# Performance work log

Measured on AMD Instinct MI355X. Metric: run time of the kernel, lower is better.

## Reference

```python
import jax, jax.numpy as jnp
import numpy as np

N_NODES = 100000
N_EDGES = 1600000
IN_FEATS = 512
HIDDEN = 128
N_CLASSES = 2
N_LAYERS = 2
NEG_SLOPE = 0.01  # F.leaky_relu default


def setup_inputs() -> dict:
    key = jax.random.key(0)
    ks = jax.random.split(key, 12)
    features = jax.random.normal(ks[0], (N_NODES, IN_FEATS), dtype=jnp.float32)
    src = jax.random.randint(ks[1], (N_EDGES,), 0, N_NODES, dtype=jnp.int32)
    dst = jax.random.randint(ks[2], (N_EDGES,), 0, N_NODES, dtype=jnp.int32)
    # params (torch Linear convention: W is [out, in], y = x @ W.T + b)
    s_in = 1.0 / np.sqrt(IN_FEATS)
    s_h = 1.0 / np.sqrt(HIDDEN)
    W_in = jax.random.uniform(ks[3], (HIDDEN, IN_FEATS), jnp.float32, -s_in, s_in)
    b_in = jax.random.uniform(ks[4], (HIDDEN,), jnp.float32, -s_in, s_in)
    # SAGEConv per layer: fc_self (with bias) + fc_neigh (no bias), stacked over layers
    W_self = jax.random.uniform(ks[5], (N_LAYERS, HIDDEN, HIDDEN), jnp.float32, -s_h, s_h)
    b_self = jax.random.uniform(ks[6], (N_LAYERS, HIDDEN), jnp.float32, -s_h, s_h)
    W_neigh = jax.random.uniform(ks[7], (N_LAYERS, HIDDEN, HIDDEN), jnp.float32, -s_h, s_h)
    W_out = jax.random.uniform(ks[8], (N_CLASSES, HIDDEN), jnp.float32, -s_h, s_h)
    b_out = jax.random.uniform(ks[9], (N_CLASSES,), jnp.float32, -s_h, s_h)
    return {
        "features": features, "src": src, "dst": dst,
        "W_in": W_in, "b_in": b_in,
        "W_self": W_self, "b_self": b_self, "W_neigh": W_neigh,
        "W_out": W_out, "b_out": b_out,
    }


def reference(features, src, dst, W_in, b_in, W_self, b_self, W_neigh, W_out, b_out):
    # input projection (dropout is identity in eval / p=0)
    h = features @ W_in.T + b_in  # [N, H]
    # in-degree for mean aggregation (zero-degree nodes -> zero neighbor feat)
    deg = jax.ops.segment_sum(jnp.ones((src.shape[0],), h.dtype), dst,
                              num_segments=N_NODES)
    inv_deg = (1.0 / jnp.maximum(deg, 1.0))[:, None]  # [N, 1]
    for l in range(N_LAYERS):
        # mean over in-neighbors: scatter-add h[src] onto dst, divide by degree
        h_neigh = jax.ops.segment_sum(h[src], dst, num_segments=N_NODES) * inv_deg
        h = h @ W_self[l].T + b_self[l] + h_neigh @ W_neigh[l].T
        h = jax.nn.leaky_relu(h, negative_slope=NEG_SLOPE)
    return h @ W_out.T + b_out  # [N, n_classes]
```

## Files before the change

### kernel.cpp

```cpp
#include <hip/hip_runtime.h>


#define N_NODES 100000
#define N_EDGES 1600000
#define IN_FEATS 512
#define HIDDEN 128
#define NEG_SLOPE 0.01f
#define SCAN_BLOCKS 49

#define N_RANGES 8
#define RANGE_SZ 12500
#define FILL_CHUNKS 256
#define FILL_CHUNK 6250

typedef __attribute__((ext_vector_type(8))) __bf16 bf16x8;
typedef __attribute__((ext_vector_type(4))) float f32x4;
typedef __attribute__((ext_vector_type(8))) _Float16 half8;

__global__ __launch_bounds__(256) void k_degree(const int* __restrict__ dst,
                                                int* __restrict__ deg) {
  int r = blockIdx.x & 7;
  int c = blockIdx.x >> 3;
  int lo = r * RANGE_SZ, hi = lo + RANGE_SZ;
  int e0 = c * FILL_CHUNK;
  int e1 = e0 + FILL_CHUNK;
  if (e1 > N_EDGES) e1 = N_EDGES;
  for (int e = e0 + threadIdx.x; e < e1; e += 256) {
    int d = dst[e];
    if (d >= lo && d < hi) atomicAdd(&deg[d], 1);
  }
}

__device__ __forceinline__ int wave_incl_scan(int v) {
  #pragma unroll
  for (int d = 1; d < 64; d <<= 1) {
    int t = __shfl_up(v, d, 64);
    if ((threadIdx.x & 63) >= d) v += t;
  }
  return v;
}

__global__ __launch_bounds__(256) void k_scanA(const int* __restrict__ deg,
                                               int* __restrict__ out,
                                               int* __restrict__ bsums) {
  __shared__ int wsum[4];
  int base = blockIdx.x * 2048 + threadIdx.x * 8;
  int v[8];
  int s = 0;
  #pragma unroll
  for (int i = 0; i < 8; i++) {
    int idx = base + i;
    v[i] = (idx < N_NODES) ? deg[idx] : 0;
    s += v[i];
  }
  int incl = wave_incl_scan(s);
  int wid = threadIdx.x >> 6;
  if ((threadIdx.x & 63) == 63) wsum[wid] = incl;
  __syncthreads();
  int woff = 0;
  #pragma unroll
  for (int w = 0; w < 4; w++)
    if (w < wid) woff += wsum[w];
  int run = woff + incl - s;
  #pragma unroll
  for (int i = 0; i < 8; i++) {
    int idx = base + i;
    if (idx < N_NODES) out[idx] = run;
    run += v[i];
  }
  if (threadIdx.x == 255) bsums[blockIdx.x] = woff + incl;
}

__global__ __launch_bounds__(64) void k_scanB(const int* __restrict__ bsums,
                                              int* __restrict__ boffs) {
  int t = threadIdx.x;
  int v = (t < SCAN_BLOCKS) ? bsums[t] : 0;
  int incl = wave_incl_scan(v);
  if (t < SCAN_BLOCKS) boffs[t] = incl - v;
}

__global__ __launch_bounds__(256) void k_scanC(const int* __restrict__ deg,
                                               int* __restrict__ row_start,
                                               int* __restrict__ cursor,
                                               float* __restrict__ inv_deg,
                                               const int* __restrict__ boffs) {
  int b = boffs[blockIdx.x];
  int base = blockIdx.x * 2048 + threadIdx.x * 8;
  #pragma unroll
  for (int i = 0; i < 8; i++) {
    int idx = base + i;
    if (idx < N_NODES) {
      int rs = row_start[idx] + b;
      row_start[idx] = rs;
      cursor[idx] = rs;
      int d = deg[idx];
      inv_deg[idx] = 1.0f / (float)(d > 1 ? d : 1);
    }
  }
  if (blockIdx.x == 0 && threadIdx.x == 0) row_start[N_NODES] = N_EDGES;
}

__global__ __launch_bounds__(256) void k_fill(const int* __restrict__ src,
                                              const int* __restrict__ dst,
                                              int* __restrict__ cursor,
                                              int* __restrict__ csr_src) {
  int r = blockIdx.x & 7;
  int c = blockIdx.x >> 3;
  int lo = r * RANGE_SZ, hi = lo + RANGE_SZ;
  int e0 = c * FILL_CHUNK;
  int e1 = e0 + FILL_CHUNK;
  if (e1 > N_EDGES) e1 = N_EDGES;
  for (int e = e0 + threadIdx.x; e < e1; e += 256) {
    int d = dst[e];
    if (d >= lo && d < hi) {
      int p = atomicAdd(&cursor[d], 1);
      csr_src[p] = src[e];
    }
  }
}

template <int K1, int K2, bool RELU, bool WF16>
__global__ __launch_bounds__(256) void k_gemm(const float* __restrict__ A1,
                                              const float* __restrict__ A2,
                                              const float* __restrict__ W1,
                                              const float* __restrict__ W2,
                                              const float* __restrict__ bias,
                                              float* __restrict__ C,
                                              _Float16* __restrict__ C16) {
  constexpr int BK = 32;
  constexpr int KT = (K1 + K2) / BK;
  constexpr int LP = 40;
  __shared__ __bf16 As_h[128 * LP];
  __shared__ __bf16 As_l[128 * LP];
  __shared__ __bf16 Bs_h[128 * LP];
  __shared__ __bf16 Bs_l[128 * LP];

  const int tid = threadIdx.x;
  const int lane = tid & 63;
  const int wid = tid >> 6;
  const int wr = wid >> 1;
  const int wc = wid & 1;
  const int lr = lane & 15;
  const int kg = lane >> 4;
  const int r0 = blockIdx.x * 128;

  f32x4 acc[4][4];
  #pragma unroll
  for (int m = 0; m < 4; m++)
    #pragma unroll
    for (int n = 0; n < 4; n++) acc[m][n] = (f32x4){0.f, 0.f, 0.f, 0.f};

  float4 ra[4], rb[4];

  auto load_tile = [&](int kt) {
    const float* Ap;
    const float* Wp;
    int k0, lda;
    if (K2 == 0 || kt * BK < K1) {
      Ap = A1; Wp = W1; k0 = kt * BK; lda = K1;
    } else {
      Ap = A2; Wp = W2; k0 = kt * BK - K1; lda = K2;
    }
    #pragma unroll
    for (int i = 0; i < 4; i++) {
      int flat = i * 256 + tid;
      int row = flat >> 3;
      int q = flat & 7;
      int gr = r0 + row;
      ra[i] = (gr < N_NODES) ? *(const float4*)&Ap[(long)gr * lda + k0 + q * 4]
                             : make_float4(0.f, 0.f, 0.f, 0.f);
      rb[i] = *(const float4*)&Wp[(long)row * lda + k0 + q * 4];
    }
  };

  auto split_write = [&](float v, __bf16* hp, __bf16* lp, int off) {
    __bf16 h = (__bf16)v;
    float rem = v - (float)h;
    hp[off] = h;
    lp[off] = (__bf16)rem;
  };

  load_tile(0);

  for (int kt = 0; kt < KT; ++kt) {
    if (kt > 0) __syncthreads();
    #pragma unroll
    for (int i = 0; i < 4; i++) {
      int flat = i * 256 + tid;
      int row = flat >> 3;
      int q = flat & 7;
      int off = row * LP + q * 4;
      split_write(ra[i].x, As_h, As_l, off + 0);
      split_write(ra[i].y, As_h, As_l, off + 1);
      split_write(ra[i].z, As_h, As_l, off + 2);
      split_write(ra[i].w, As_h, As_l, off + 3);
      split_write(rb[i].x, Bs_h, Bs_l, off + 0);
      split_write(rb[i].y, Bs_h, Bs_l, off + 1);
      split_write(rb[i].z, Bs_h, Bs_l, off + 2);
      split_write(rb[i].w, Bs_h, Bs_l, off + 3);
    }
    __syncthreads();
    if (kt + 1 < KT) load_tile(kt + 1);

    bf16x8 ah[4], al[4];
    #pragma unroll
    for (int m = 0; m < 4; m++) {
      int arow = wr * 64 + m * 16 + lr;
      ah[m] = *(const bf16x8*)&As_h[arow * LP + kg * 8];
      al[m] = *(const bf16x8*)&As_l[arow * LP + kg * 8];
    }
    #pragma unroll
    for (int n = 0; n < 4; n++) {
      int bcol = wc * 64 + n * 16 + lr;
      bf16x8 bh = *(const bf16x8*)&Bs_h[bcol * LP + kg * 8];
      bf16x8 bl = *(const bf16x8*)&Bs_l[bcol * LP + kg * 8];
      #pragma unroll
      for (int m = 0; m < 4; m++) {
        acc[m][n] = __builtin_amdgcn_mfma_f32_16x16x32_bf16(ah[m], bh, acc[m][n], 0, 0, 0);
        acc[m][n] = __builtin_amdgcn_mfma_f32_16x16x32_bf16(al[m], bh, acc[m][n], 0, 0, 0);
        acc[m][n] = __builtin_amdgcn_mfma_f32_16x16x32_bf16(ah[m], bl, acc[m][n], 0, 0, 0);
      }
    }
  }

  #pragma unroll
  for (int n = 0; n < 4; n++) {
    int col = wc * 64 + n * 16 + lr;
    float bc = bias[col];
    #pragma unroll
    for (int m = 0; m < 4; m++) {
      int rowb = r0 + wr * 64 + m * 16 + kg * 4;
      #pragma unroll
      for (int j = 0; j < 4; j++) {
        int row = rowb + j;
        if (row < N_NODES) {
          float v = acc[m][n][j] + bc;
          if (RELU) v = v > 0.f ? v : v * NEG_SLOPE;
          C[(long)row * 128 + col] = v;
          if (WF16) C16[(long)row * 128 + col] = (_Float16)v;
        }
      }
    }
  }
}

__global__ __launch_bounds__(256) void k_agg(const _Float16* __restrict__ h16,
                                             const int* __restrict__ row_start,
                                             const int* __restrict__ csr_src,
                                             const float* __restrict__ inv_deg,
                                             float* __restrict__ hn) {
  int node = blockIdx.x * 16 + (threadIdx.x >> 4);
  int lane = threadIdx.x & 15;
  int s = row_start[node];
  int e = row_start[node + 1];
  float acc[8];
  #pragma unroll
  for (int j = 0; j < 8; j++) acc[j] = 0.f;

  int i = s;
  for (; i + 4 <= e; i += 4) {
    int s0 = csr_src[i + 0];
    int s1 = csr_src[i + 1];
    int s2 = csr_src[i + 2];
    int s3 = csr_src[i + 3];
    half8 v0 = *(const half8*)&h16[(long)s0 * HIDDEN + lane * 8];
    half8 v1 = *(const half8*)&h16[(long)s1 * HIDDEN + lane * 8];
    half8 v2 = *(const half8*)&h16[(long)s2 * HIDDEN + lane * 8];
    half8 v3 = *(const half8*)&h16[(long)s3 * HIDDEN + lane * 8];
    #pragma unroll
    for (int j = 0; j < 8; j++)
      acc[j] += ((float)v0[j] + (float)v1[j]) + ((float)v2[j] + (float)v3[j]);
  }
  for (; i < e; ++i) {
    int sn = csr_src[i];
    half8 v = *(const half8*)&h16[(long)sn * HIDDEN + lane * 8];
    #pragma unroll
    for (int j = 0; j < 8; j++) acc[j] += (float)v[j];
  }

  float id = inv_deg[node];
  float4 o0, o1;
  o0.x = acc[0] * id; o0.y = acc[1] * id; o0.z = acc[2] * id; o0.w = acc[3] * id;
  o1.x = acc[4] * id; o1.y = acc[5] * id; o1.z = acc[6] * id; o1.w = acc[7] * id;
  *(float4*)&hn[(long)node * HIDDEN + lane * 8 + 0] = o0;
  *(float4*)&hn[(long)node * HIDDEN + lane * 8 + 4] = o1;
}

__global__ __launch_bounds__(256) void k_out(const float* __restrict__ h,
                                             const float* __restrict__ W_out,
                                             const float* __restrict__ b_out,
                                             float* __restrict__ out) {
  int node = blockIdx.x * 4 + (threadIdx.x >> 6);
  int l = threadIdx.x & 63;
  float a = h[node * HIDDEN + l];
  float b = h[node * HIDDEN + 64 + l];
  float s0 = a * W_out[l] + b * W_out[64 + l];
  float s1 = a * W_out[128 + l] + b * W_out[192 + l];
  #pragma unroll
  for (int d = 32; d >= 1; d >>= 1) {
    s0 += __shfl_xor(s0, d, 64);
    s1 += __shfl_xor(s1, d, 64);
  }
  if (l == 0) {
    out[node * 2 + 0] = s0 + b_out[0];
    out[node * 2 + 1] = s1 + b_out[1];
  }
}

extern "C" void kernel_launch(void* const* d_in, const int* in_sizes, int n_in,
                              void* d_out, int out_size, void* d_ws, size_t ws_size,
                              hipStream_t stream) {
  const float* features = (const float*)d_in[0];
  const int* src = (const int*)d_in[1];
  const int* dst = (const int*)d_in[2];
  const float* W_in = (const float*)d_in[3];
  const float* b_in = (const float*)d_in[4];
  const float* W_self = (const float*)d_in[5];
  const float* b_self = (const float*)d_in[6];
  const float* W_neigh = (const float*)d_in[7];
  const float* W_out = (const float*)d_in[8];
  const float* b_out = (const float*)d_in[9];
  float* out = (float*)d_out;

  char* ws = (char*)d_ws;
  float* h = (float*)(ws + 0);
  float* hn = (float*)(ws + 51200000);
  int* deg = (int*)(ws + 102400000);
  float* inv_deg = (float*)(ws + 102800000);
  int* row_start = (int*)(ws + 103200000);
  int* cursor = (int*)(ws + 103600016);
  int* csr_src = (int*)(ws + 104000016);
  int* bsums = (int*)(ws + 110400016);
  int* boffs = (int*)(ws + 110400272);
  _Float16* h16 = (_Float16*)(ws + 110401024);

  hipMemsetAsync(deg, 0, N_NODES * sizeof(int), stream);
  k_degree<<<N_RANGES * FILL_CHUNKS, 256, 0, stream>>>(dst, deg);
  k_scanA<<<SCAN_BLOCKS, 256, 0, stream>>>(deg, row_start, bsums);
  k_scanB<<<1, 64, 0, stream>>>(bsums, boffs);
  k_scanC<<<SCAN_BLOCKS, 256, 0, stream>>>(deg, row_start, cursor, inv_deg, boffs);
  k_fill<<<N_RANGES * FILL_CHUNKS, 256, 0, stream>>>(src, dst, cursor, csr_src);

  k_gemm<IN_FEATS, 0, false, true><<<782, 256, 0, stream>>>(
      features, nullptr, W_in, nullptr, b_in, h, h16);

  k_agg<<<6250, 256, 0, stream>>>(h16, row_start, csr_src, inv_deg, hn);
  k_gemm<HIDDEN, HIDDEN, true, true><<<782, 256, 0, stream>>>(
      h, hn, W_self, W_neigh, b_self, h, h16);

  k_agg<<<6250, 256, 0, stream>>>(h16, row_start, csr_src, inv_deg, hn);
  k_gemm<HIDDEN, HIDDEN, true, false><<<782, 256, 0, stream>>>(
      h, hn, W_self + HIDDEN * HIDDEN, W_neigh + HIDDEN * HIDDEN,
      b_self + HIDDEN, h, nullptr);

  k_out<<<25000, 256, 0, stream>>>(h, W_out, b_out, out);
}
```

Baseline: 722.7 us.

## Pre-split weights and activations into bf16 hi/lo and load MFMA fragments directly

Measured after the change: 870.1 us. 1.2x slower.

```diff
diff --git a/kernel.cpp b/kernel.cpp
--- a/kernel.cpp
+++ b/kernel.cpp
@@ -14,6 +14,7 @@
 #define FILL_CHUNK 6250
 
 typedef __attribute__((ext_vector_type(8))) __bf16 bf16x8;
+typedef __attribute__((ext_vector_type(4))) __bf16 bf16x4;
 typedef __attribute__((ext_vector_type(4))) float f32x4;
 typedef __attribute__((ext_vector_type(8))) _Float16 half8;
 
@@ -119,108 +120,122 @@
   }
 }
 
-template <int K1, int K2, bool RELU, bool WF16>
-__global__ __launch_bounds__(256) void k_gemm(const float* __restrict__ A1,
-                                              const float* __restrict__ A2,
-                                              const float* __restrict__ W1,
-                                              const float* __restrict__ W2,
-                                              const float* __restrict__ bias,
-                                              float* __restrict__ C,
-                                              _Float16* __restrict__ C16) {
+__global__ __launch_bounds__(256) void k_split(const float* __restrict__ in,
+                                               __bf16* __restrict__ hi,
+                                               __bf16* __restrict__ lo, int n) {
+  int i = (blockIdx.x * 256 + threadIdx.x) * 4;
+  if (i >= n) return;
+  float4 v = *(const float4*)&in[i];
+  float vv[4] = {v.x, v.y, v.z, v.w};
+  bf16x4 h4, l4;
+  #pragma unroll
+  for (int j = 0; j < 4; j++) {
+    __bf16 hh = (__bf16)vv[j];
+    h4[j] = hh;
+    l4[j] = (__bf16)(vv[j] - (float)hh);
+  }
+  *(bf16x4*)&hi[i] = h4;
+  *(bf16x4*)&lo[i] = l4;
+}
+
+template <int K1, int K2, bool RELU, bool A16, bool WF32, bool WSPLIT, bool WF16>
+__global__ __launch_bounds__(256, 2) void k_gemm(
+    const void* __restrict__ A1a, const void* __restrict__ A1b,
+    const void* __restrict__ A2a, const void* __restrict__ A2b,
+    const __bf16* __restrict__ W1h, const __bf16* __restrict__ W1l,
+    const __bf16* __restrict__ W2h, const __bf16* __restrict__ W2l,
+    const float* __restrict__ bias,
+    float* __restrict__ Cf, __bf16* __restrict__ Ch, __bf16* __restrict__ Cl,
+    _Float16* __restrict__ C16) {
+  static_assert(K2 == 0 || K2 == K1, "uniform lda required");
   constexpr int BK = 32;
   constexpr int KT = (K1 + K2) / BK;
-  constexpr int LP = 40;
-  __shared__ __bf16 As_h[128 * LP];
-  __shared__ __bf16 As_l[128 * LP];
-  __shared__ __bf16 Bs_h[128 * LP];
-  __shared__ __bf16 Bs_l[128 * LP];
-
   const int tid = threadIdx.x;
   const int lane = tid & 63;
   const int wid = tid >> 6;
-  const int wr = wid >> 1;
-  const int wc = wid & 1;
-  const int lr = lane & 15;
-  const int kg = lane >> 4;
+  const int wr = wid >> 1, wc = wid & 1;
+  const int lr = lane & 15, kg = lane >> 4;
   const int r0 = blockIdx.x * 128;
 
+  long abase[4];
+  long bbase[4];
+  #pragma unroll
+  for (int m = 0; m < 4; m++) {
+    int r = r0 + wr * 64 + m * 16 + lr;
+    int rc = (r < N_NODES) ? r : (N_NODES - 1);
+    abase[m] = (long)rc * K1;
+    bbase[m] = (long)(wc * 64 + m * 16 + lr) * K1;
+  }
+
   f32x4 acc[4][4];
   #pragma unroll
   for (int m = 0; m < 4; m++)
     #pragma unroll
     for (int n = 0; n < 4; n++) acc[m][n] = (f32x4){0.f, 0.f, 0.f, 0.f};
 
-  float4 ra[4], rb[4];
-
-  auto load_tile = [&](int kt) {
-    const float* Ap;
-    const float* Wp;
-    int k0, lda;
-    if (K2 == 0 || kt * BK < K1) {
-      Ap = A1; Wp = W1; k0 = kt * BK; lda = K1;
+  float4 af[4][2];
+  bf16x8 sah[4], sal[4];
+  bf16x8 sbh[4], sbl[4];
+  bf16x8 ah[4], al[4], bh[4], bl[4];
+
+  auto issue = [&](int kt) {
+    const bool fst = (K2 == 0) || (kt * BK < K1);
+    const int k0 = (fst ? kt * BK : kt * BK - K1) + kg * 8;
+    if constexpr (A16) {
+      const __bf16* Ah = (const __bf16*)(fst ? A1a : A2a);
+      const __bf16* Al = (const __bf16*)(fst ? A1b : A2b);
+      #pragma unroll
+      for (int m = 0; m < 4; m++) {
+        sah[m] = *(const bf16x8*)&Ah[abase[m] + k0];
+        sal[m] = *(const bf16x8*)&Al[abase[m] + k0];
+      }
     } else {
-      Ap = A2; Wp = W2; k0 = kt * BK - K1; lda = K2;
-    }
-    #pragma unroll
-    for (int i = 0; i < 4; i++) {
-      int flat = i * 256 + tid;
-      int row = flat >> 3;
-      int q = flat & 7;
-      int gr = r0 + row;
-      ra[i] = (gr < N_NODES) ? *(const float4*)&Ap[(long)gr * lda + k0 + q * 4]
-                             : make_float4(0.f, 0.f, 0.f, 0.f);
-      rb[i] = *(const float4*)&Wp[(long)row * lda + k0 + q * 4];
+      const float* Af = (const float*)(fst ? A1a : A2a);
+      #pragma unroll
+      for (int m = 0; m < 4; m++) {
+        af[m][0] = *(const float4*)&Af[abase[m] + k0];
+        af[m][1] = *(const float4*)&Af[abase[m] + k0 + 4];
+      }
+    }
+    const __bf16* Bh = fst ? W1h : W2h;
+    const __bf16* Bl = fst ? W1l : W2l;
+    #pragma unroll
+    for (int n = 0; n < 4; n++) {
+      sbh[n] = *(const bf16x8*)&Bh[bbase[n] + k0];
+      sbl[n] = *(const bf16x8*)&Bl[bbase[n] + k0];
     }
   };
 
-  auto split_write = [&](float v, __bf16* hp, __bf16* lp, int off) {
-    __bf16 h = (__bf16)v;
-    float rem = v - (float)h;
-    hp[off] = h;
-    lp[off] = (__bf16)rem;
-  };
-
-  load_tile(0);
-
+  issue(0);
+  #pragma unroll 4
   for (int kt = 0; kt < KT; ++kt) {
-    if (kt > 0) __syncthreads();
-    #pragma unroll
-    for (int i = 0; i < 4; i++) {
-      int flat = i * 256 + tid;
-      int row = flat >> 3;
-      int q = flat & 7;
-      int off = row * LP + q * 4;
-      split_write(ra[i].x, As_h, As_l, off + 0);
-      split_write(ra[i].y, As_h, As_l, off + 1);
-      split_write(ra[i].z, As_h, As_l, off + 2);
-      split_write(ra[i].w, As_h, As_l, off + 3);
-      split_write(rb[i].x, Bs_h, Bs_l, off + 0);
-      split_write(rb[i].y, Bs_h, Bs_l, off + 1);
-      split_write(rb[i].z, Bs_h, Bs_l, off + 2);
-      split_write(rb[i].w, Bs_h, Bs_l, off + 3);
-    }
-    __syncthreads();
-    if (kt + 1 < KT) load_tile(kt + 1);
-
-    bf16x8 ah[4], al[4];
-    #pragma unroll
-    for (int m = 0; m < 4; m++) {
-      int arow = wr * 64 + m * 16 + lr;
-      ah[m] = *(const bf16x8*)&As_h[arow * LP + kg * 8];
-      al[m] = *(const bf16x8*)&As_l[arow * LP + kg * 8];
-    }
-    #pragma unroll
-    for (int n = 0; n < 4; n++) {
-      int bcol = wc * 64 + n * 16 + lr;
-      bf16x8 bh = *(const bf16x8*)&Bs_h[bcol * LP + kg * 8];
-      bf16x8 bl = *(const bf16x8*)&Bs_l[bcol * LP + kg * 8];
+    if constexpr (A16) {
+      #pragma unroll
+      for (int m = 0; m < 4; m++) { ah[m] = sah[m]; al[m] = sal[m]; }
+    } else {
       #pragma unroll
       for (int m = 0; m < 4; m++) {
-        acc[m][n] = __builtin_amdgcn_mfma_f32_16x16x32_bf16(ah[m], bh, acc[m][n], 0, 0, 0);
-        acc[m][n] = __builtin_amdgcn_mfma_f32_16x16x32_bf16(al[m], bh, acc[m][n], 0, 0, 0);
-        acc[m][n] = __builtin_amdgcn_mfma_f32_16x16x32_bf16(ah[m], bl, acc[m][n], 0, 0, 0);
+        float v[8] = {af[m][0].x, af[m][0].y, af[m][0].z, af[m][0].w,
+                      af[m][1].x, af[m][1].y, af[m][1].z, af[m][1].w};
+        #pragma unroll
+        for (int j = 0; j < 8; j++) {
+          __bf16 hh = (__bf16)v[j];
+          ah[m][j] = hh;
+          al[m][j] = (__bf16)(v[j] - (float)hh);
+        }
       }
     }
+    #pragma unroll
+    for (int n = 0; n < 4; n++) { bh[n] = sbh[n]; bl[n] = sbl[n]; }
+    if (kt + 1 < KT) issue(kt + 1);
+    #pragma unroll
+    for (int n = 0; n < 4; n++)
+      #pragma unroll
+      for (int m = 0; m < 4; m++) {
+        acc[m][n] = __builtin_amdgcn_mfma_f32_16x16x32_bf16(ah[m], bh[n], acc[m][n], 0, 0, 0);
+        acc[m][n] = __builtin_amdgcn_mfma_f32_16x16x32_bf16(al[m], bh[n], acc[m][n], 0, 0, 0);
+        acc[m][n] = __builtin_amdgcn_mfma_f32_16x16x32_bf16(ah[m], bl[n], acc[m][n], 0, 0, 0);
+      }
   }
 
   #pragma unroll
@@ -236,8 +251,14 @@
         if (row < N_NODES) {
           float v = acc[m][n][j] + bc;
           if (RELU) v = v > 0.f ? v : v * NEG_SLOPE;
-          C[(long)row * 128 + col] = v;
-          if (WF16) C16[(long)row * 128 + col] = (_Float16)v;
+          long o = (long)row * 128 + col;
+          if (WF32) Cf[o] = v;
+          if (WSPLIT) {
+            __bf16 hh = (__bf16)v;
+            Ch[o] = hh;
+            Cl[o] = (__bf16)(v - (float)hh);
+          }
+          if (WF16) C16[o] = (_Float16)v;
         }
       }
     }
@@ -248,7 +269,8 @@
                                              const int* __restrict__ row_start,
                                              const int* __restrict__ csr_src,
                                              const float* __restrict__ inv_deg,
-                                             float* __restrict__ hn) {
+                                             __bf16* __restrict__ hn_h,
+                                             __bf16* __restrict__ hn_l) {
   int node = blockIdx.x * 16 + (threadIdx.x >> 4);
   int lane = threadIdx.x & 15;
   int s = row_start[node];
@@ -279,11 +301,16 @@
   }
 
   float id = inv_deg[node];
-  float4 o0, o1;
-  o0.x = acc[0] * id; o0.y = acc[1] * id; o0.z = acc[2] * id; o0.w = acc[3] * id;
-  o1.x = acc[4] * id; o1.y = acc[5] * id; o1.z = acc[6] * id; o1.w = acc[7] * id;
-  *(float4*)&hn[(long)node * HIDDEN + lane * 8 + 0] = o0;
-  *(float4*)&hn[(long)node * HIDDEN + lane * 8 + 4] = o1;
+  bf16x8 oh, ol;
+  #pragma unroll
+  for (int j = 0; j < 8; j++) {
+    float v = acc[j] * id;
+    __bf16 hh = (__bf16)v;
+    oh[j] = hh;
+    ol[j] = (__bf16)(v - (float)hh);
+  }
+  *(bf16x8*)&hn_h[(long)node * HIDDEN + lane * 8] = oh;
+  *(bf16x8*)&hn_l[(long)node * HIDDEN + lane * 8] = ol;
 }
 
 __global__ __launch_bounds__(256) void k_out(const float* __restrict__ h,
@@ -324,15 +351,24 @@
 
   char* ws = (char*)d_ws;
   float* h = (float*)(ws + 0);
-  float* hn = (float*)(ws + 51200000);
-  int* deg = (int*)(ws + 102400000);
-  float* inv_deg = (float*)(ws + 102800000);
-  int* row_start = (int*)(ws + 103200000);
-  int* cursor = (int*)(ws + 103600016);
-  int* csr_src = (int*)(ws + 104000016);
-  int* bsums = (int*)(ws + 110400016);
-  int* boffs = (int*)(ws + 110400272);
-  _Float16* h16 = (_Float16*)(ws + 110401024);
+  _Float16* h16 = (_Float16*)(ws + 51200000);
+  __bf16* h_hi = (__bf16*)(ws + 76800000);
+  __bf16* h_lo = (__bf16*)(ws + 102400000);
+  __bf16* hn_h = (__bf16*)(ws + 128000000);
+  __bf16* hn_l = (__bf16*)(ws + 153600000);
+  int* deg = (int*)(ws + 179200000);
+  float* inv_deg = (float*)(ws + 179600000);
+  int* row_start = (int*)(ws + 180000000);
+  int* cursor = (int*)(ws + 180400016);
+  int* csr_src = (int*)(ws + 180800016);
+  int* bsums = (int*)(ws + 187200016);
+  int* boffs = (int*)(ws + 187200272);
+  __bf16* W_in_h = (__bf16*)(ws + 187201024);
+  __bf16* W_in_l = (__bf16*)(ws + 187332096);
+  __bf16* W_sf_h = (__bf16*)(ws + 187463168);
+  __bf16* W_sf_l = (__bf16*)(ws + 187528704);
+  __bf16* W_ng_h = (__bf16*)(ws + 187594240);
+  __bf16* W_ng_l = (__bf16*)(ws + 187659776);
 
   hipMemsetAsync(deg, 0, N_NODES * sizeof(int), stream);
   k_degree<<<N_RANGES * FILL_CHUNKS, 256, 0, stream>>>(dst, deg);
@@ -341,17 +377,24 @@
   k_scanC<<<SCAN_BLOCKS, 256, 0, stream>>>(deg, row_start, cursor, inv_deg, boffs);
   k_fill<<<N_RANGES * FILL_CHUNKS, 256, 0, stream>>>(src, dst, cursor, csr_src);
 
-  k_gemm<IN_FEATS, 0, false, true><<<782, 256, 0, stream>>>(
-      features, nullptr, W_in, nullptr, b_in, h, h16);
-
-  k_agg<<<6250, 256, 0, stream>>>(h16, row_start, csr_src, inv_deg, hn);
-  k_gemm<HIDDEN, HIDDEN, true, true><<<782, 256, 0, stream>>>(
-      h, hn, W_self, W_neigh, b_self, h, h16);
-
-  k_agg<<<6250, 256, 0, stream>>>(h16, row_start, csr_src, inv_deg, hn);
-  k_gemm<HIDDEN, HIDDEN, true, false><<<782, 256, 0, stream>>>(
-      h, hn, W_self + HIDDEN * HIDDEN, W_neigh + HIDDEN * HIDDEN,
-      b_self + HIDDEN, h, nullptr);
+  k_split<<<64, 256, 0, stream>>>(W_in, W_in_h, W_in_l, IN_FEATS * HIDDEN);
+  k_split<<<32, 256, 0, stream>>>(W_self, W_sf_h, W_sf_l, 2 * HIDDEN * HIDDEN);
+  k_split<<<32, 256, 0, stream>>>(W_neigh, W_ng_h, W_ng_l, 2 * HIDDEN * HIDDEN);
+
+  k_gemm<IN_FEATS, 0, false, false, false, true, true><<<782, 256, 0, stream>>>(
+      features, nullptr, nullptr, nullptr, W_in_h, W_in_l, nullptr, nullptr,
+      b_in, nullptr, h_hi, h_lo, h16);
+
+  k_agg<<<6250, 256, 0, stream>>>(h16, row_start, csr_src, inv_deg, hn_h, hn_l);
+  k_gemm<HIDDEN, HIDDEN, true, true, false, true, true><<<782, 256, 0, stream>>>(
+      h_hi, h_lo, hn_h, hn_l, W_sf_h, W_sf_l, W_ng_h, W_ng_l,
+      b_self, nullptr, h_hi, h_lo, h16);
+
+  k_agg<<<6250, 256, 0, stream>>>(h16, row_start, csr_src, inv_deg, hn_h, hn_l);
+  k_gemm<HIDDEN, HIDDEN, true, true, true, false, false><<<782, 256, 0, stream>>>(
+      h_hi, h_lo, hn_h, hn_l, W_sf_h + HIDDEN * HIDDEN, W_sf_l + HIDDEN * HIDDEN,
+      W_ng_h + HIDDEN * HIDDEN, W_ng_l + HIDDEN * HIDDEN,
+      b_self + HIDDEN, h, nullptr, nullptr, nullptr);
 
   k_out<<<25000, 256, 0, stream>>>(h, W_out, b_out, out);
 }
```
